# Kernel tuning notes

Measured on AMD Instinct MI355X. Metric: run time of the kernel, lower is better.

Reference implementation:

```python
import jax, jax.numpy as jnp
import numpy as np

EMBED_DIM = 1024
PROJ_DIM = 64
B, S = 8, 2048


def setup_inputs() -> dict:
    key = jax.random.key(0)
    k1, k2, k3 = jax.random.split(key, 3)
    context = jax.random.normal(k1, (S, B, EMBED_DIM), dtype=jnp.float32)
    prior = jax.random.uniform(k2, (B, S), dtype=jnp.float32)
    # xavier_uniform for (2*proj_dim, embed_dim)
    bound = float(np.sqrt(6.0 / (2 * PROJ_DIM + EMBED_DIM)))
    proj_weight = jax.random.uniform(k3, (2 * PROJ_DIM, EMBED_DIM), dtype=jnp.float32,
                                     minval=-bound, maxval=bound)
    proj_bias = jnp.zeros((2 * PROJ_DIM,), dtype=jnp.float32)
    return {"context": context, "prior": prior,
            "proj_weight": proj_weight, "proj_bias": proj_bias}


def reference(context, prior, proj_weight, proj_bias):
    # context: (S, B, E) -> (B, S, E)
    x = jnp.transpose(context, (1, 0, 2))
    b, s, e = x.shape
    qk = jnp.einsum('bse,pe->bsp', x, proj_weight) + proj_bias  # (B,S,2P)
    query, key = jnp.split(qk, 2, axis=2)
    # neighbor scores, scaled by embed_dim (as in the original)
    fwd = jnp.sum(query[:, :-1] * key[:, 1:], axis=-1) / e   # (B,S-1) score i<->i+1
    bwd = jnp.sum(query[:, 1:] * key[:, :-1], axis=-1) / e   # (B,S-1) score i<->i-1
    ninf = jnp.full((b, 1), -jnp.inf, dtype=x.dtype)
    score = jnp.stack([jnp.concatenate([fwd, ninf], axis=1),
                       jnp.concatenate([ninf, bwd], axis=1)], axis=-1)  # (B,S,2)
    prob = jax.nn.softmax(score, axis=-1)
    # torch .roll(shifts=-1) with no dims flattens the whole tensor: reproduce that
    shift_prob = jnp.roll(prob[:, :, 1].reshape(-1), -1).reshape(b, s)
    prob0 = jnp.sqrt(prob[:, :, 0] * shift_prob + 1e-6)      # (B,S)
    neighbor_attn = prior + (1.0 - prior) * prob0
    log_prob = jnp.log(neighbor_attn)
    # Original places log_prob[:, :-1] on the superdiagonal and hits it with
    # triu matmuls on both sides: C[i,j] = sum_{m=i}^{j-1} log_prob[m] for j>i.
    # Equivalent O(n^2): prefix sums cs[t] = sum_{m<t} log_prob[m].
    cs = jnp.concatenate([jnp.zeros((b, 1), dtype=x.dtype),
                          jnp.cumsum(log_prob[:, :-1], axis=1)], axis=1)  # (B,S)
    D = cs[:, None, :] - cs[:, :, None]            # D[b,i,j] = cs[j]-cs[i]
    i_idx = jnp.arange(s)
    upper = i_idx[None, :] > i_idx[:, None]        # (S,S) j>i
    M = jnp.where(upper[None], D, -D)              # C + C^T (symmetric)
    constituent_attn = jnp.exp(M)
    diag = i_idx[None, :] == i_idx[:, None]
    constituent_attn = jnp.where(diag[None], jnp.zeros((), x.dtype), constituent_attn)
    return constituent_attn, neighbor_attn
```

## Files before the change

kernel.cpp:

```cpp
#include <hip/hip_runtime.h>
#include <cstdint>
#include <cstddef>

#define E_DIM 1024
#define PD 64
#define NP 128
#define B_DIM 8
#define S_DIM 2048
#define M_TOT (B_DIM * S_DIM)

#define BMR 32
#define BK 32
#define NCH (E_DIM / BK)

typedef __attribute__((ext_vector_type(8))) short short8v;
typedef __attribute__((ext_vector_type(4))) float f32x4;

__device__ __forceinline__ void gload16(const void* g, void* l) {
    __builtin_amdgcn_global_load_lds(
        (const __attribute__((address_space(1))) unsigned int*)g,
        (__attribute__((address_space(3))) unsigned int*)(uintptr_t)l,
        16, 0, 0);
}

__device__ __forceinline__ void cvt_hilo(const f32x4 v0, const f32x4 v1,
                                         short8v& h, short8v& l) {
    const unsigned MSK = 0xFFFF0000u;
    unsigned a0 = __float_as_uint(v0.x), a1 = __float_as_uint(v0.y);
    unsigned a2 = __float_as_uint(v0.z), a3 = __float_as_uint(v0.w);
    unsigned a4 = __float_as_uint(v1.x), a5 = __float_as_uint(v1.y);
    unsigned a6 = __float_as_uint(v1.z), a7 = __float_as_uint(v1.w);
    float l0 = v0.x - __uint_as_float(a0 & MSK);
    float l1 = v0.y - __uint_as_float(a1 & MSK);
    float l2 = v0.z - __uint_as_float(a2 & MSK);
    float l3 = v0.w - __uint_as_float(a3 & MSK);
    float l4 = v1.x - __uint_as_float(a4 & MSK);
    float l5 = v1.y - __uint_as_float(a5 & MSK);
    float l6 = v1.z - __uint_as_float(a6 & MSK);
    float l7 = v1.w - __uint_as_float(a7 & MSK);
    union { unsigned u[4]; short8v s; } H, L;
    H.u[0] = (a1 & MSK) | (a0 >> 16);
    H.u[1] = (a3 & MSK) | (a2 >> 16);
    H.u[2] = (a5 & MSK) | (a4 >> 16);
    H.u[3] = (a7 & MSK) | (a6 >> 16);
    L.u[0] = (__float_as_uint(l1) & MSK) | (__float_as_uint(l0) >> 16);
    L.u[1] = (__float_as_uint(l3) & MSK) | (__float_as_uint(l2) >> 16);
    L.u[2] = (__float_as_uint(l5) & MSK) | (__float_as_uint(l4) >> 16);
    L.u[3] = (__float_as_uint(l7) & MSK) | (__float_as_uint(l6) >> 16);
    h = H.s; l = L.s;
}

__global__ __launch_bounds__(256) void conv_w(const float* __restrict__ W,
                                              ushort* __restrict__ hiImg,
                                              ushort* __restrict__ loImg) {
    const int t = blockIdx.x * 256 + threadIdx.x;
    const int c  = t & 127;
    const int q  = (t >> 7) & 3;
    const int ch = t >> 9;
    const float* src = W + (size_t)c * E_DIM + ch * 32 + q * 8;
    const f32x4 v0 = *(const f32x4*)src;
    const f32x4 v1 = *(const f32x4*)(src + 4);
    short8v h, l;
    cvt_hilo(v0, v1, h, l);
    const size_t off = ((size_t)(ch * 4 + q) * NP + c) * 8;
    *(short8v*)&hiImg[off] = h;
    *(short8v*)&loImg[off] = l;
}

__global__ __launch_bounds__(256, 2) void gemm_qk(const float* __restrict__ A,
                                                  const ushort* __restrict__ hiImg,
                                                  const ushort* __restrict__ loImg,
                                                  const float* __restrict__ bias,
                                                  float* __restrict__ qk) {
    __shared__ __align__(16) float  As[2][BMR][BK];
    __shared__ __align__(16) ushort Whi[2][4][NP][8];
    __shared__ __align__(16) ushort Wlo[2][4][NP][8];
    const int tid = threadIdx.x;
    const int m0  = blockIdx.x * BMR;
    const int w   = __builtin_amdgcn_readfirstlane(tid >> 6);
    const int ln  = tid & 63;
    const int lr  = ln >> 3;
    const int g8  = ln & 7;
    const int row16 = ln & 15;
    const int kq    = ln >> 4;
    const int r7    = row16 & 7;
    const int sg0 = ((((kq << 1) | 0) ^ r7) & 7) << 2;
    const int sg1 = ((((kq << 1) | 1) ^ r7) & 7) << 2;

    const float*  aS = A + (size_t)(m0 + w * 8 + lr) * E_DIM + ((g8 ^ lr) << 2);
    const ushort* hS = hiImg + (size_t)(w * 2) * 512 + ln * 8;
    const ushort* lS = loImg + (size_t)(w * 2) * 512 + ln * 8;

    float bias2[2];
    bias2[0] = bias[w * 32 + row16];
    bias2[1] = bias[w * 32 + 16 + row16];

    f32x4 acc[2][2];
#pragma unroll
    for (int i = 0; i < 2; ++i)
#pragma unroll
        for (int j = 0; j < 2; ++j) acc[i][j] = (f32x4){0.f, 0.f, 0.f, 0.f};

#define STAGE(BUF, CH)                                                          \
    {                                                                           \
        gload16(aS + (size_t)(CH) * BK, &As[BUF][w * 8][0]);                    \
        gload16(hS + (size_t)(CH) * 4096,       (ushort*)Whi[BUF] + (w * 2) * 512);       \
        gload16(hS + (size_t)(CH) * 4096 + 512, (ushort*)Whi[BUF] + (w * 2 + 1) * 512);   \
        gload16(lS + (size_t)(CH) * 4096,       (ushort*)Wlo[BUF] + (w * 2) * 512);       \
        gload16(lS + (size_t)(CH) * 4096 + 512, (ushort*)Wlo[BUF] + (w * 2 + 1) * 512);   \
    }

    STAGE(0, 0)

    for (int ch = 0; ch < NCH; ++ch) {
        const int buf = ch & 1;
        __syncthreads();
        if (ch + 1 < NCH) {
            STAGE(buf ^ 1, ch + 1)
        }
        short8v ah[2], al[2];
#pragma unroll
        for (int fi = 0; fi < 2; ++fi) {
            const float* base = &As[buf][fi * 16 + row16][0];
            const f32x4 v0 = *(const f32x4*)(base + sg0);
            const f32x4 v1 = *(const f32x4*)(base + sg1);
            cvt_hilo(v0, v1, ah[fi], al[fi]);
        }
        short8v wh[2], wl[2];
#pragma unroll
        for (int fj = 0; fj < 2; ++fj) {
            wh[fj] = *(const short8v*)&Whi[buf][kq][w * 32 + fj * 16 + row16][0];
            wl[fj] = *(const short8v*)&Wlo[buf][kq][w * 32 + fj * 16 + row16][0];
        }
#pragma unroll
        for (int fi = 0; fi < 2; ++fi)
#pragma unroll
            for (int fj = 0; fj < 2; ++fj) {
                acc[fi][fj] = __builtin_amdgcn_mfma_f32_16x16x32_bf16(
                    ah[fi], wh[fj], acc[fi][fj], 0, 0, 0);
                acc[fi][fj] = __builtin_amdgcn_mfma_f32_16x16x32_bf16(
                    ah[fi], wl[fj], acc[fi][fj], 0, 0, 0);
                acc[fi][fj] = __builtin_amdgcn_mfma_f32_16x16x32_bf16(
                    al[fi], wh[fj], acc[fi][fj], 0, 0, 0);
            }
    }
#undef STAGE

#pragma unroll
    for (int fi = 0; fi < 2; ++fi)
#pragma unroll
        for (int fj = 0; fj < 2; ++fj) {
#pragma unroll
            for (int r = 0; r < 4; ++r) {
                const int m = m0 + fi * 16 + kq * 4 + r;
                const int p = w * 32 + fj * 16 + row16;
                qk[(size_t)m * NP + p] = acc[fi][fj][r] + bias2[fj];
            }
        }
}

__global__ __launch_bounds__(256) void neighbor_probs(const float* __restrict__ qk,
                                                      float* __restrict__ p0,
                                                      float* __restrict__ p1) {
    const int m = blockIdx.x * 4 + (threadIdx.x >> 6);
    const int lane = threadIdx.x & 63;
    const int s = m >> 3;
    const int b = m & 7;

    const float q = qk[(size_t)m * NP + lane];
    const float kn = (s < S_DIM - 1) ? qk[(size_t)(m + B_DIM) * NP + PD + lane] : 0.f;
    const float kp = (s > 0) ? qk[(size_t)(m - B_DIM) * NP + PD + lane] : 0.f;
    float f = q * kn;
    float g = q * kp;
#pragma unroll
    for (int off = 32; off; off >>= 1) {
        f += __shfl_xor(f, off);
        g += __shfl_xor(g, off);
    }
    if (lane == 0) {
        const float s0 = f * (1.f / (float)E_DIM);
        const float s1 = g * (1.f / (float)E_DIM);
        float P0, P1;
        if (s == S_DIM - 1) { P0 = 0.f; P1 = 1.f; }
        else if (s == 0)    { P0 = 1.f; P1 = 0.f; }
        else {
            const float mx = fmaxf(s0, s1);
            const float e0 = __expf(s0 - mx), e1 = __expf(s1 - mx);
            const float inv = 1.f / (e0 + e1);
            P0 = e0 * inv; P1 = e1 * inv;
        }
        p0[b * S_DIM + s] = P0;
        p1[b * S_DIM + s] = P1;
    }
}

__global__ __launch_bounds__(256) void combine_scan(const float* __restrict__ p0,
                                                    const float* __restrict__ p1,
                                                    const float* __restrict__ prior,
                                                    float* __restrict__ out_na,
                                                    float* __restrict__ cs) {
    const int b = blockIdx.x;
    const int tid = threadIdx.x;
    __shared__ float sh[256];

    const int base = b * S_DIM + tid * 8;
    float incl[8];
    float run = 0.f;
#pragma unroll
    for (int u = 0; u < 8; ++u) {
        const int fidx = base + u;
        int nf = fidx + 1;
        if (nf == B_DIM * S_DIM) nf = 0;
        const float P0 = p0[fidx];
        const float sp = p1[nf];
        const float pr = prior[fidx];
        const float na = pr + (1.f - pr) * sqrtf(P0 * sp + 1e-6f);
        out_na[fidx] = na;
        run += __logf(na);
        incl[u] = run;
    }
    sh[tid] = run;
    __syncthreads();
    for (int off = 1; off < 256; off <<= 1) {
        float v = sh[tid];
        if (tid >= off) v += sh[tid - off];
        __syncthreads();
        sh[tid] = v;
        __syncthreads();
    }
    const float offset = (tid > 0) ? sh[tid - 1] : 0.f;
#pragma unroll
    for (int u = 0; u < 8; ++u) {
        cs[base + u] = offset + ((u > 0) ? incl[u - 1] : 0.f);
    }
}

__global__ __launch_bounds__(256) void big_out(const float* __restrict__ cs,
                                               float* __restrict__ out) {
    const int bi = blockIdx.x;
    const int b = bi >> 11;
    const int i = bi & (S_DIM - 1);
    const float ci = cs[b * S_DIM + i];
    const float* crow = cs + (size_t)b * S_DIM;
    float* orow = out + (size_t)bi * S_DIM;
    const int j0 = threadIdx.x * 8;
#pragma unroll
    for (int h = 0; h < 2; ++h) {
        const int j = j0 + h * 4;
        const f32x4 cj = *(const f32x4*)&crow[j];
        f32x4 o;
        {
            const int jj = j + 0; const float m = (jj > i) ? (cj.x - ci) : (ci - cj.x);
            o.x = (jj == i) ? 0.f : __expf(m);
        }
        {
            const int jj = j + 1; const float m = (jj > i) ? (cj.y - ci) : (ci - cj.y);
            o.y = (jj == i) ? 0.f : __expf(m);
        }
        {
            const int jj = j + 2; const float m = (jj > i) ? (cj.z - ci) : (ci - cj.z);
            o.z = (jj == i) ? 0.f : __expf(m);
        }
        {
            const int jj = j + 3; const float m = (jj > i) ? (cj.w - ci) : (ci - cj.w);
            o.w = (jj == i) ? 0.f : __expf(m);
        }
        *(f32x4*)&orow[j] = o;
    }
}

extern "C" void kernel_launch(void* const* d_in, const int* in_sizes, int n_in,
                              void* d_out, int out_size, void* d_ws, size_t ws_size,
                              hipStream_t stream) {
    const float* context = (const float*)d_in[0];
    const float* prior   = (const float*)d_in[1];
    const float* W       = (const float*)d_in[2];
    const float* bias    = (const float*)d_in[3];
    float* out = (float*)d_out;

    float* qk = (float*)d_ws;
    float* p0 = qk + (size_t)M_TOT * NP;
    float* p1 = p0 + M_TOT;
    float* cs = p1 + M_TOT;
    ushort* hiImg = (ushort*)out;
    ushort* loImg = hiImg + (size_t)NP * E_DIM;
    float* na_out = out + (size_t)B_DIM * S_DIM * S_DIM;

    conv_w<<<64, 256, 0, stream>>>(W, hiImg, loImg);
    gemm_qk<<<M_TOT / BMR, 256, 0, stream>>>(context, hiImg, loImg, bias, qk);
    neighbor_probs<<<M_TOT / 4, 256, 0, stream>>>(qk, p0, p1);
    combine_scan<<<B_DIM, 256, 0, stream>>>(p0, p1, prior, na_out, cs);
    big_out<<<M_TOT, 256, 0, stream>>>(cs, out);
}
```

Baseline: 64.49 us.

## Load weight images straight to registers and stage A through registers

Swaps the LDS-DMA (global_load_lds) double buffering for register prefetching. The hi/lo weight fragments are now read from global memory straight into registers two chunks ahead. A rows are loaded into registers and written by hand into a swizzled LDS double buffer. This drops the weight LDS arrays and their LDS reads, which lowers LDS traffic and footprint. The cost is more registers, manual waitcnt/sched barriers, and weight loads that each wave repeats from global memory (L2), with the usual risks of hand-written synchronisation.

```diff
diff --git a/kernel.cpp b/kernel.cpp
--- a/kernel.cpp
+++ b/kernel.cpp
@@ -15,13 +15,6 @@
 
 typedef __attribute__((ext_vector_type(8))) short short8v;
 typedef __attribute__((ext_vector_type(4))) float f32x4;
-
-__device__ __forceinline__ void gload16(const void* g, void* l) {
-    __builtin_amdgcn_global_load_lds(
-        (const __attribute__((address_space(1))) unsigned int*)g,
-        (__attribute__((address_space(3))) unsigned int*)(uintptr_t)l,
-        16, 0, 0);
-}
 
 __device__ __forceinline__ void cvt_hilo(const f32x4 v0, const f32x4 v1,
                                          short8v& h, short8v& l) {
@@ -72,12 +65,10 @@
                                                   const ushort* __restrict__ loImg,
                                                   const float* __restrict__ bias,
                                                   float* __restrict__ qk) {
-    __shared__ __align__(16) float  As[2][BMR][BK];
-    __shared__ __align__(16) ushort Whi[2][4][NP][8];
-    __shared__ __align__(16) ushort Wlo[2][4][NP][8];
+    __shared__ __align__(16) float As[2][BMR][BK];
     const int tid = threadIdx.x;
     const int m0  = blockIdx.x * BMR;
-    const int w   = __builtin_amdgcn_readfirstlane(tid >> 6);
+    const int w   = tid >> 6;
     const int ln  = tid & 63;
     const int lr  = ln >> 3;
     const int g8  = ln & 7;
@@ -87,9 +78,11 @@
     const int sg0 = ((((kq << 1) | 0) ^ r7) & 7) << 2;
     const int sg1 = ((((kq << 1) | 1) ^ r7) & 7) << 2;
 
-    const float*  aS = A + (size_t)(m0 + w * 8 + lr) * E_DIM + ((g8 ^ lr) << 2);
-    const ushort* hS = hiImg + (size_t)(w * 2) * 512 + ln * 8;
-    const ushort* lS = loImg + (size_t)(w * 2) * 512 + ln * 8;
+    const float* aS = A + (size_t)(m0 + w * 8 + lr) * E_DIM + (g8 << 2);
+    float* const aDst0 = &As[0][0][0] + (w * 8 + lr) * BK + ((g8 ^ lr) << 2);
+    float* const aDst1 = &As[1][0][0] + (w * 8 + lr) * BK + ((g8 ^ lr) << 2);
+    const ushort* hS = hiImg + ((size_t)kq * NP + w * 32 + row16) * 8;
+    const ushort* lS = loImg + ((size_t)kq * NP + w * 32 + row16) * 8;
 
     float bias2[2];
     bias2[0] = bias[w * 32 + row16];
@@ -101,50 +94,69 @@
 #pragma unroll
         for (int j = 0; j < 2; ++j) acc[i][j] = (f32x4){0.f, 0.f, 0.f, 0.f};
 
-#define STAGE(BUF, CH)                                                          \
-    {                                                                           \
-        gload16(aS + (size_t)(CH) * BK, &As[BUF][w * 8][0]);                    \
-        gload16(hS + (size_t)(CH) * 4096,       (ushort*)Whi[BUF] + (w * 2) * 512);       \
-        gload16(hS + (size_t)(CH) * 4096 + 512, (ushort*)Whi[BUF] + (w * 2 + 1) * 512);   \
-        gload16(lS + (size_t)(CH) * 4096,       (ushort*)Wlo[BUF] + (w * 2) * 512);       \
-        gload16(lS + (size_t)(CH) * 4096 + 512, (ushort*)Wlo[BUF] + (w * 2 + 1) * 512);   \
-    }
-
-    STAGE(0, 0)
-
-    for (int ch = 0; ch < NCH; ++ch) {
-        const int buf = ch & 1;
-        __syncthreads();
-        if (ch + 1 < NCH) {
-            STAGE(buf ^ 1, ch + 1)
-        }
-        short8v ah[2], al[2];
-#pragma unroll
-        for (int fi = 0; fi < 2; ++fi) {
-            const float* base = &As[buf][fi * 16 + row16][0];
-            const f32x4 v0 = *(const f32x4*)(base + sg0);
-            const f32x4 v1 = *(const f32x4*)(base + sg1);
-            cvt_hilo(v0, v1, ah[fi], al[fi]);
-        }
-        short8v wh[2], wl[2];
-#pragma unroll
-        for (int fj = 0; fj < 2; ++fj) {
-            wh[fj] = *(const short8v*)&Whi[buf][kq][w * 32 + fj * 16 + row16][0];
-            wl[fj] = *(const short8v*)&Wlo[buf][kq][w * 32 + fj * 16 + row16][0];
-        }
-#pragma unroll
-        for (int fi = 0; fi < 2; ++fi)
-#pragma unroll
-            for (int fj = 0; fj < 2; ++fj) {
-                acc[fi][fj] = __builtin_amdgcn_mfma_f32_16x16x32_bf16(
-                    ah[fi], wh[fj], acc[fi][fj], 0, 0, 0);
-                acc[fi][fj] = __builtin_amdgcn_mfma_f32_16x16x32_bf16(
-                    ah[fi], wl[fj], acc[fi][fj], 0, 0, 0);
-                acc[fi][fj] = __builtin_amdgcn_mfma_f32_16x16x32_bf16(
-                    al[fi], wh[fj], acc[fi][fj], 0, 0, 0);
-            }
-    }
-#undef STAGE
+    f32x4 aP0, aP1;
+    short8v wh00, wh01, wl00, wl01;
+    short8v wh10, wh11, wl10, wl11;
+
+    aP0 = *(const f32x4*)(aS);
+    aP1 = *(const f32x4*)(aS + BK);
+    wh00 = *(const short8v*)(hS);
+    wh01 = *(const short8v*)(hS + 128);
+    wl00 = *(const short8v*)(lS);
+    wl01 = *(const short8v*)(lS + 128);
+    wh10 = *(const short8v*)(hS + 4096);
+    wh11 = *(const short8v*)(hS + 4096 + 128);
+    wl10 = *(const short8v*)(lS + 4096);
+    wl11 = *(const short8v*)(lS + 4096 + 128);
+    *(f32x4*)aDst0 = aP0;
+    asm volatile("s_waitcnt lgkmcnt(0)" ::: "memory");
+    __builtin_amdgcn_sched_barrier(0);
+
+#define GBODY(P, CH, APcur, APother, WH0, WH1, WL0, WL1, DSTother, SRCbuf)          \
+    {                                                                               \
+        __builtin_amdgcn_s_barrier();                                               \
+        __builtin_amdgcn_sched_barrier(0);                                          \
+        if ((CH) + 1 < NCH) { *(f32x4*)(DSTother) = APother; }                      \
+        if ((CH) + 2 < NCH) {                                                       \
+            APcur = *(const f32x4*)(aS + ((CH) + 2) * BK);                          \
+        }                                                                           \
+        short8v ah0, al0, ah1, al1;                                                 \
+        {                                                                           \
+            const float* b0 = &As[SRCbuf][row16][0];                                \
+            cvt_hilo(*(const f32x4*)(b0 + sg0), *(const f32x4*)(b0 + sg1), ah0, al0); \
+            const float* b1 = &As[SRCbuf][16 + row16][0];                           \
+            cvt_hilo(*(const f32x4*)(b1 + sg0), *(const f32x4*)(b1 + sg1), ah1, al1); \
+        }                                                                           \
+        acc[0][0] = __builtin_amdgcn_mfma_f32_16x16x32_bf16(ah0, WH0, acc[0][0], 0, 0, 0); \
+        acc[0][0] = __builtin_amdgcn_mfma_f32_16x16x32_bf16(ah0, WL0, acc[0][0], 0, 0, 0); \
+        acc[0][0] = __builtin_amdgcn_mfma_f32_16x16x32_bf16(al0, WH0, acc[0][0], 0, 0, 0); \
+        acc[0][1] = __builtin_amdgcn_mfma_f32_16x16x32_bf16(ah0, WH1, acc[0][1], 0, 0, 0); \
+        acc[0][1] = __builtin_amdgcn_mfma_f32_16x16x32_bf16(ah0, WL1, acc[0][1], 0, 0, 0); \
+        acc[0][1] = __builtin_amdgcn_mfma_f32_16x16x32_bf16(al0, WH1, acc[0][1], 0, 0, 0); \
+        acc[1][0] = __builtin_amdgcn_mfma_f32_16x16x32_bf16(ah1, WH0, acc[1][0], 0, 0, 0); \
+        acc[1][0] = __builtin_amdgcn_mfma_f32_16x16x32_bf16(ah1, WL0, acc[1][0], 0, 0, 0); \
+        acc[1][0] = __builtin_amdgcn_mfma_f32_16x16x32_bf16(al1, WH0, acc[1][0], 0, 0, 0); \
+        acc[1][1] = __builtin_amdgcn_mfma_f32_16x16x32_bf16(ah1, WH1, acc[1][1], 0, 0, 0); \
+        acc[1][1] = __builtin_amdgcn_mfma_f32_16x16x32_bf16(ah1, WL1, acc[1][1], 0, 0, 0); \
+        acc[1][1] = __builtin_amdgcn_mfma_f32_16x16x32_bf16(al1, WH1, acc[1][1], 0, 0, 0); \
+        if ((CH) + 2 < NCH) {                                                       \
+            WH0 = *(const short8v*)(hS + (size_t)((CH) + 2) * 4096);                \
+            WH1 = *(const short8v*)(hS + (size_t)((CH) + 2) * 4096 + 128);          \
+            WL0 = *(const short8v*)(lS + (size_t)((CH) + 2) * 4096);                \
+            WL1 = *(const short8v*)(lS + (size_t)((CH) + 2) * 4096 + 128);          \
+        }                                                                           \
+        asm volatile("s_waitcnt lgkmcnt(0)" ::: "memory");                          \
+        __builtin_amdgcn_sched_barrier(0);                                          \
+    }
+
+#pragma unroll 1
+    for (int c2 = 0; c2 < NCH / 2; ++c2) {
+        const int ch0 = 2 * c2;
+        GBODY(0, ch0, aP0, aP1, wh00, wh01, wl00, wl01, aDst1, 0)
+        const int ch1 = 2 * c2 + 1;
+        GBODY(1, ch1, aP1, aP0, wh10, wh11, wl10, wl11, aDst0, 1)
+    }
+#undef GBODY
 
 #pragma unroll
     for (int fi = 0; fi < 2; ++fi)
```

Result: slower. 66.23 us (+2.7%).

## Fuse all stages into one cooperative persistent kernel with grid syncs

Applied to the files above, without the earlier changes.

Replaces the five separate launches (weight conversion, GEMM, neighbor probs, scan, big output) with a single cooperative kernel of 512 blocks separated by grid.sync. The GEMM tile now loads 48 rows (with 8-row halos) so neighbor dot products are computed from LDS without writing the full qk matrix to global memory. Weights are read directly from global into registers instead of LDS staging, and the output phase caches the cs row in LDS with each block writing 32 rows. This trades launch overhead and qk round-trips for redundant halo GEMM work, grid-wide barriers, and an only partly occupied scan phase.

```diff
diff --git a/kernel.cpp b/kernel.cpp
--- a/kernel.cpp
+++ b/kernel.cpp
@@ -1,6 +1,9 @@
 #include <hip/hip_runtime.h>
+#include <hip/hip_cooperative_groups.h>
 #include <cstdint>
 #include <cstddef>
+
+namespace cg = cooperative_groups;
 
 #define E_DIM 1024
 #define PD 64
@@ -9,9 +12,9 @@
 #define S_DIM 2048
 #define M_TOT (B_DIM * S_DIM)
 
-#define BMR 32
 #define BK 32
 #define NCH (E_DIM / BK)
+#define GRID 512
 
 typedef __attribute__((ext_vector_type(8))) short short8v;
 typedef __attribute__((ext_vector_type(4))) float f32x4;
@@ -50,222 +53,240 @@
     h = H.s; l = L.s;
 }
 
-__global__ __launch_bounds__(256) void conv_w(const float* __restrict__ W,
-                                              ushort* __restrict__ hiImg,
-                                              ushort* __restrict__ loImg) {
-    const int t = blockIdx.x * 256 + threadIdx.x;
-    const int c  = t & 127;
-    const int q  = (t >> 7) & 3;
-    const int ch = t >> 9;
-    const float* src = W + (size_t)c * E_DIM + ch * 32 + q * 8;
-    const f32x4 v0 = *(const f32x4*)src;
-    const f32x4 v1 = *(const f32x4*)(src + 4);
-    short8v h, l;
-    cvt_hilo(v0, v1, h, l);
-    const size_t off = ((size_t)(ch * 4 + q) * NP + c) * 8;
-    *(short8v*)&hiImg[off] = h;
-    *(short8v*)&loImg[off] = l;
-}
-
-__global__ __launch_bounds__(256, 2) void gemm_qk(const float* __restrict__ A,
-                                                  const ushort* __restrict__ hiImg,
-                                                  const ushort* __restrict__ loImg,
-                                                  const float* __restrict__ bias,
-                                                  float* __restrict__ qk) {
-    __shared__ __align__(16) float  As[2][BMR][BK];
-    __shared__ __align__(16) ushort Whi[2][4][NP][8];
-    __shared__ __align__(16) ushort Wlo[2][4][NP][8];
+#define MFMA(d, a, b) d = __builtin_amdgcn_mfma_f32_16x16x32_bf16(a, b, d, 0, 0, 0)
+
+__global__ __launch_bounds__(256, 2) void fused_all(const float* __restrict__ A,
+                                                    const float* __restrict__ W,
+                                                    const float* __restrict__ prior,
+                                                    const float* __restrict__ bias,
+                                                    float* __restrict__ out,
+                                                    void* __restrict__ ws) {
+    __shared__ __align__(16) union {
+        struct { float As[2][48][BK]; float Cmat[48][132]; } b;
+        float csL[S_DIM];
+        float scan[256];
+    } sh;
+
+    ushort* hiImg = (ushort*)ws;
+    ushort* loImg = hiImg + (size_t)NP * E_DIM;
+    float*  wsf   = (float*)ws;
+    float*  p0    = wsf + 131072;
+    float*  p1    = p0 + M_TOT;
+    float*  cs    = p1 + M_TOT;
+    float*  na_out = out + (size_t)B_DIM * S_DIM * S_DIM;
+
     const int tid = threadIdx.x;
-    const int m0  = blockIdx.x * BMR;
-    const int w   = __builtin_amdgcn_readfirstlane(tid >> 6);
-    const int ln  = tid & 63;
-    const int lr  = ln >> 3;
-    const int g8  = ln & 7;
-    const int row16 = ln & 15;
-    const int kq    = ln >> 4;
-    const int r7    = row16 & 7;
-    const int sg0 = ((((kq << 1) | 0) ^ r7) & 7) << 2;
-    const int sg1 = ((((kq << 1) | 1) ^ r7) & 7) << 2;
-
-    const float*  aS = A + (size_t)(m0 + w * 8 + lr) * E_DIM + ((g8 ^ lr) << 2);
-    const ushort* hS = hiImg + (size_t)(w * 2) * 512 + ln * 8;
-    const ushort* lS = loImg + (size_t)(w * 2) * 512 + ln * 8;
-
-    float bias2[2];
-    bias2[0] = bias[w * 32 + row16];
-    bias2[1] = bias[w * 32 + 16 + row16];
-
-    f32x4 acc[2][2];
-#pragma unroll
-    for (int i = 0; i < 2; ++i)
-#pragma unroll
-        for (int j = 0; j < 2; ++j) acc[i][j] = (f32x4){0.f, 0.f, 0.f, 0.f};
-
-#define STAGE(BUF, CH)                                                          \
-    {                                                                           \
-        gload16(aS + (size_t)(CH) * BK, &As[BUF][w * 8][0]);                    \
-        gload16(hS + (size_t)(CH) * 4096,       (ushort*)Whi[BUF] + (w * 2) * 512);       \
-        gload16(hS + (size_t)(CH) * 4096 + 512, (ushort*)Whi[BUF] + (w * 2 + 1) * 512);   \
-        gload16(lS + (size_t)(CH) * 4096,       (ushort*)Wlo[BUF] + (w * 2) * 512);       \
-        gload16(lS + (size_t)(CH) * 4096 + 512, (ushort*)Wlo[BUF] + (w * 2 + 1) * 512);   \
+    const int g   = blockIdx.x;
+    cg::grid_group grid = cg::this_grid();
+
+    {
+        const int t = g * 256 + tid;
+        if (t < NP * E_DIM / 8) {
+            const int c  = t & 127;
+            const int q  = (t >> 7) & 3;
+            const int ch = t >> 9;
+            const float* src = W + (size_t)c * E_DIM + ch * 32 + q * 8;
+            const f32x4 v0 = *(const f32x4*)src;
+            const f32x4 v1 = *(const f32x4*)(src + 4);
+            short8v h, l;
+            cvt_hilo(v0, v1, h, l);
+            const size_t off = ((size_t)(ch * 4 + q) * NP + c) * 8;
+            *(short8v*)&hiImg[off] = h;
+            *(short8v*)&loImg[off] = l;
+        }
     }
-
-    STAGE(0, 0)
-
-    for (int ch = 0; ch < NCH; ++ch) {
-        const int buf = ch & 1;
+    grid.sync();
+
+    {
+        const int m0 = g * 32;
+        const int w  = tid >> 6;
+        const int ln = tid & 63;
+        const int lr = ln >> 3;
+        const int g8 = ln & 7;
+        const int row16 = ln & 15;
+        const int kq    = ln >> 4;
+        const int r7    = row16 & 7;
+        const int sg0 = ((((kq << 1) | 0) ^ r7) & 7) << 2;
+        const int sg1 = ((((kq << 1) | 1) ^ r7) & 7) << 2;
+
+        long gr1 = (long)m0 - 8 + w * 8 + lr;
+        gr1 = gr1 < 0 ? 0 : (gr1 >= M_TOT ? M_TOT - 1 : gr1);
+        const float* aP1 = A + (size_t)gr1 * E_DIM + ((g8 ^ lr) << 2);
+        const float* aP2 = aP1;
+        if (w < 2) {
+            long gr2 = (long)m0 - 8 + 32 + w * 8 + lr;
+            gr2 = gr2 < 0 ? 0 : (gr2 >= M_TOT ? M_TOT - 1 : gr2);
+            aP2 = A + (size_t)gr2 * E_DIM + ((g8 ^ lr) << 2);
+        }
+        const ushort* hS = hiImg + ((size_t)kq * NP + w * 32 + row16) * 8;
+        const ushort* lS = loImg + ((size_t)kq * NP + w * 32 + row16) * 8;
+        float bias2[2];
+        bias2[0] = bias[w * 32 + row16];
+        bias2[1] = bias[w * 32 + 16 + row16];
+
+        f32x4 acc[3][2];
+#pragma unroll
+        for (int i = 0; i < 3; ++i)
+#pragma unroll
+            for (int j = 0; j < 2; ++j) acc[i][j] = (f32x4){0.f, 0.f, 0.f, 0.f};
+
+        short8v whA0, whA1, wlA0, wlA1, whB0, whB1, wlB0, wlB1;
+
+        gload16(aP1, &sh.b.As[0][w * 8][0]);
+        if (w < 2) gload16(aP2, &sh.b.As[0][32 + w * 8][0]);
+        whA0 = *(const short8v*)(hS);
+        whA1 = *(const short8v*)(hS + 128);
+        wlA0 = *(const short8v*)(lS);
+        wlA1 = *(const short8v*)(lS + 128);
+
+#define GB(CH, WH0, WH1, WL0, WL1, NWH0, NWH1, NWL0, NWL1)                          \
+        {                                                                           \
+            const int buf = (CH) & 1;                                               \
+            __syncthreads();                                                        \
+            if ((CH) + 1 < NCH) {                                                   \
+                gload16(aP1 + ((CH) + 1) * BK, &sh.b.As[buf ^ 1][w * 8][0]);        \
+                if (w < 2) gload16(aP2 + ((CH) + 1) * BK, &sh.b.As[buf ^ 1][32 + w * 8][0]); \
+                NWH0 = *(const short8v*)(hS + (size_t)((CH) + 1) * 4096);           \
+                NWH1 = *(const short8v*)(hS + (size_t)((CH) + 1) * 4096 + 128);     \
+                NWL0 = *(const short8v*)(lS + (size_t)((CH) + 1) * 4096);           \
+                NWL1 = *(const short8v*)(lS + (size_t)((CH) + 1) * 4096 + 128);     \
+            }                                                                       \
+            short8v ah, al;                                                         \
+            _Pragma("unroll")                                                       \
+            for (int rf = 0; rf < 3; ++rf) {                                        \
+                const float* bp = &sh.b.As[buf][rf * 16 + row16][0];                \
+                cvt_hilo(*(const f32x4*)(bp + sg0), *(const f32x4*)(bp + sg1), ah, al); \
+                MFMA(acc[rf][0], ah, WH0);                                          \
+                MFMA(acc[rf][0], ah, WL0);                                          \
+                MFMA(acc[rf][0], al, WH0);                                          \
+                MFMA(acc[rf][1], ah, WH1);                                          \
+                MFMA(acc[rf][1], ah, WL1);                                          \
+                MFMA(acc[rf][1], al, WH1);                                          \
+            }                                                                       \
+        }
+
+#pragma unroll 1
+        for (int c2 = 0; c2 < NCH / 2; ++c2) {
+            GB(2 * c2,     whA0, whA1, wlA0, wlA1, whB0, whB1, wlB0, wlB1)
+            GB(2 * c2 + 1, whB0, whB1, wlB0, wlB1, whA0, whA1, wlA0, wlA1)
+        }
+#undef GB
+
         __syncthreads();
-        if (ch + 1 < NCH) {
-            STAGE(buf ^ 1, ch + 1)
-        }
-        short8v ah[2], al[2];
-#pragma unroll
-        for (int fi = 0; fi < 2; ++fi) {
-            const float* base = &As[buf][fi * 16 + row16][0];
-            const f32x4 v0 = *(const f32x4*)(base + sg0);
-            const f32x4 v1 = *(const f32x4*)(base + sg1);
-            cvt_hilo(v0, v1, ah[fi], al[fi]);
-        }
-        short8v wh[2], wl[2];
-#pragma unroll
-        for (int fj = 0; fj < 2; ++fj) {
-            wh[fj] = *(const short8v*)&Whi[buf][kq][w * 32 + fj * 16 + row16][0];
-            wl[fj] = *(const short8v*)&Wlo[buf][kq][w * 32 + fj * 16 + row16][0];
-        }
-#pragma unroll
-        for (int fi = 0; fi < 2; ++fi)
-#pragma unroll
-            for (int fj = 0; fj < 2; ++fj) {
-                acc[fi][fj] = __builtin_amdgcn_mfma_f32_16x16x32_bf16(
-                    ah[fi], wh[fj], acc[fi][fj], 0, 0, 0);
-                acc[fi][fj] = __builtin_amdgcn_mfma_f32_16x16x32_bf16(
-                    ah[fi], wl[fj], acc[fi][fj], 0, 0, 0);
-                acc[fi][fj] = __builtin_amdgcn_mfma_f32_16x16x32_bf16(
-                    al[fi], wh[fj], acc[fi][fj], 0, 0, 0);
+#pragma unroll
+        for (int rf = 0; rf < 3; ++rf)
+#pragma unroll
+            for (int fj = 0; fj < 2; ++fj)
+#pragma unroll
+                for (int r = 0; r < 4; ++r)
+                    sh.b.Cmat[rf * 16 + kq * 4 + r][w * 32 + fj * 16 + row16] =
+                        acc[rf][fj][r] + bias2[fj];
+        __syncthreads();
+
+#pragma unroll 1
+        for (int u = 0; u < 8; ++u) {
+            const int tr = 8 + w * 8 + u;
+            const float q  = sh.b.Cmat[tr][ln];
+            const float kf = sh.b.Cmat[tr + 8][64 + ln];
+            const float kb = sh.b.Cmat[tr - 8][64 + ln];
+            float f  = q * kf;
+            float g2 = q * kb;
+#pragma unroll
+            for (int off = 32; off; off >>= 1) {
+                f  += __shfl_xor(f, off);
+                g2 += __shfl_xor(g2, off);
             }
+            if (ln == 0) {
+                const int s_abs = g * 4 + w;
+                const int bb = u;
+                float P0, P1;
+                if (s_abs == 0)             { P0 = 1.f; P1 = 0.f; }
+                else if (s_abs == S_DIM - 1){ P0 = 0.f; P1 = 1.f; }
+                else {
+                    const float s0 = f  * (1.f / (float)E_DIM);
+                    const float s1 = g2 * (1.f / (float)E_DIM);
+                    const float mx = fmaxf(s0, s1);
+                    const float e0 = __expf(s0 - mx), e1 = __expf(s1 - mx);
+                    const float inv = 1.f / (e0 + e1);
+                    P0 = e0 * inv; P1 = e1 * inv;
+                }
+                p0[bb * S_DIM + s_abs] = P0;
+                p1[bb * S_DIM + s_abs] = P1;
+            }
+        }
     }
-#undef STAGE
-
-#pragma unroll
-    for (int fi = 0; fi < 2; ++fi)
-#pragma unroll
-        for (int fj = 0; fj < 2; ++fj) {
-#pragma unroll
-            for (int r = 0; r < 4; ++r) {
-                const int m = m0 + fi * 16 + kq * 4 + r;
-                const int p = w * 32 + fj * 16 + row16;
-                qk[(size_t)m * NP + p] = acc[fi][fj][r] + bias2[fj];
+    grid.sync();
+
+    if (g < B_DIM) {
+        const int b = g;
+        const int base = b * S_DIM + tid * 8;
+        float incl[8];
+        float run = 0.f;
+#pragma unroll
+        for (int u = 0; u < 8; ++u) {
+            const int fidx = base + u;
+            int nf = fidx + 1;
+            if (nf == B_DIM * S_DIM) nf = 0;
+            const float P0 = p0[fidx];
+            const float sp = p1[nf];
+            const float pr = prior[fidx];
+            const float na = pr + (1.f - pr) * sqrtf(P0 * sp + 1e-6f);
+            na_out[fidx] = na;
+            run += __logf(na);
+            incl[u] = run;
+        }
+        sh.scan[tid] = run;
+        __syncthreads();
+        for (int off = 1; off < 256; off <<= 1) {
+            float v = sh.scan[tid];
+            if (tid >= off) v += sh.scan[tid - off];
+            __syncthreads();
+            sh.scan[tid] = v;
+            __syncthreads();
+        }
+        const float offset = (tid > 0) ? sh.scan[tid - 1] : 0.f;
+#pragma unroll
+        for (int u = 0; u < 8; ++u) {
+            cs[base + u] = offset + ((u > 0) ? incl[u - 1] : 0.f);
+        }
+    }
+    grid.sync();
+
+    {
+        const int bD = g >> 6;
+        for (int j = tid; j < S_DIM; j += 256) sh.csL[j] = cs[bD * S_DIM + j];
+        __syncthreads();
+#pragma unroll 1
+        for (int r = 0; r < 32; ++r) {
+            const int rowg = g * 32 + r;
+            const int i = rowg & (S_DIM - 1);
+            const float ci = sh.csL[i];
+            float* orow = out + (size_t)rowg * S_DIM;
+            const int j0 = tid * 8;
+#pragma unroll
+            for (int h = 0; h < 2; ++h) {
+                const int j = j0 + h * 4;
+                const f32x4 cj = *(const f32x4*)&sh.csL[j];
+                f32x4 o;
+                {
+                    const int jj = j + 0; const float m = (jj > i) ? (cj.x - ci) : (ci - cj.x);
+                    o.x = (jj == i) ? 0.f : __expf(m);
+                }
+                {
+                    const int jj = j + 1; const float m = (jj > i) ? (cj.y - ci) : (ci - cj.y);
+                    o.y = (jj == i) ? 0.f : __expf(m);
+                }
+                {
+                    const int jj = j + 2; const float m = (jj > i) ? (cj.z - ci) : (ci - cj.z);
+                    o.z = (jj == i) ? 0.f : __expf(m);
+                }
+                {
+                    const int jj = j + 3; const float m = (jj > i) ? (cj.w - ci) : (ci - cj.w);
+                    o.w = (jj == i) ? 0.f : __expf(m);
+                }
+                *(f32x4*)&orow[j] = o;
             }
         }
-}
-
-__global__ __launch_bounds__(256) void neighbor_probs(const float* __restrict__ qk,
-                                                      float* __restrict__ p0,
-                                                      float* __restrict__ p1) {
-    const int m = blockIdx.x * 4 + (threadIdx.x >> 6);
-    const int lane = threadIdx.x & 63;
-    const int s = m >> 3;
-    const int b = m & 7;
-
-    const float q = qk[(size_t)m * NP + lane];
-    const float kn = (s < S_DIM - 1) ? qk[(size_t)(m + B_DIM) * NP + PD + lane] : 0.f;
-    const float kp = (s > 0) ? qk[(size_t)(m - B_DIM) * NP + PD + lane] : 0.f;
-    float f = q * kn;
-    float g = q * kp;
-#pragma unroll
-    for (int off = 32; off; off >>= 1) {
-        f += __shfl_xor(f, off);
-        g += __shfl_xor(g, off);
-    }
-    if (lane == 0) {
-        const float s0 = f * (1.f / (float)E_DIM);
-        const float s1 = g * (1.f / (float)E_DIM);
-        float P0, P1;
-        if (s == S_DIM - 1) { P0 = 0.f; P1 = 1.f; }
-        else if (s == 0)    { P0 = 1.f; P1 = 0.f; }
-        else {
-            const float mx = fmaxf(s0, s1);
-            const float e0 = __expf(s0 - mx), e1 = __expf(s1 - mx);
-            const float inv = 1.f / (e0 + e1);
-            P0 = e0 * inv; P1 = e1 * inv;
-        }
-        p0[b * S_DIM + s] = P0;
-        p1[b * S_DIM + s] = P1;
-    }
-}
-
-__global__ __launch_bounds__(256) void combine_scan(const float* __restrict__ p0,
-                                                    const float* __restrict__ p1,
-                                                    const float* __restrict__ prior,
-                                                    float* __restrict__ out_na,
-                                                    float* __restrict__ cs) {
-    const int b = blockIdx.x;
-    const int tid = threadIdx.x;
-    __shared__ float sh[256];
-
-    const int base = b * S_DIM + tid * 8;
-    float incl[8];
-    float run = 0.f;
-#pragma unroll
-    for (int u = 0; u < 8; ++u) {
-        const int fidx = base + u;
-        int nf = fidx + 1;
-        if (nf == B_DIM * S_DIM) nf = 0;
-        const float P0 = p0[fidx];
-        const float sp = p1[nf];
-        const float pr = prior[fidx];
-        const float na = pr + (1.f - pr) * sqrtf(P0 * sp + 1e-6f);
-        out_na[fidx] = na;
-        run += __logf(na);
-        incl[u] = run;
-    }
-    sh[tid] = run;
-    __syncthreads();
-    for (int off = 1; off < 256; off <<= 1) {
-        float v = sh[tid];
-        if (tid >= off) v += sh[tid - off];
-        __syncthreads();
-        sh[tid] = v;
-        __syncthreads();
-    }
-    const float offset = (tid > 0) ? sh[tid - 1] : 0.f;
-#pragma unroll
-    for (int u = 0; u < 8; ++u) {
-        cs[base + u] = offset + ((u > 0) ? incl[u - 1] : 0.f);
-    }
-}
-
-__global__ __launch_bounds__(256) void big_out(const float* __restrict__ cs,
-                                               float* __restrict__ out) {
-    const int bi = blockIdx.x;
-    const int b = bi >> 11;
-    const int i = bi & (S_DIM - 1);
-    const float ci = cs[b * S_DIM + i];
-    const float* crow = cs + (size_t)b * S_DIM;
-    float* orow = out + (size_t)bi * S_DIM;
-    const int j0 = threadIdx.x * 8;
-#pragma unroll
-    for (int h = 0; h < 2; ++h) {
-        const int j = j0 + h * 4;
-        const f32x4 cj = *(const f32x4*)&crow[j];
-        f32x4 o;
-        {
-            const int jj = j + 0; const float m = (jj > i) ? (cj.x - ci) : (ci - cj.x);
-            o.x = (jj == i) ? 0.f : __expf(m);
-        }
-        {
-            const int jj = j + 1; const float m = (jj > i) ? (cj.y - ci) : (ci - cj.y);
-            o.y = (jj == i) ? 0.f : __expf(m);
-        }
-        {
-            const int jj = j + 2; const float m = (jj > i) ? (cj.z - ci) : (ci - cj.z);
-            o.z = (jj == i) ? 0.f : __expf(m);
-        }
-        {
-            const int jj = j + 3; const float m = (jj > i) ? (cj.w - ci) : (ci - cj.w);
-            o.w = (jj == i) ? 0.f : __expf(m);
-        }
-        *(f32x4*)&orow[j] = o;
     }
 }
 
@@ -278,17 +299,8 @@
     const float* bias    = (const float*)d_in[3];
     float* out = (float*)d_out;
 
-    float* qk = (float*)d_ws;
-    float* p0 = qk + (size_t)M_TOT * NP;
-    float* p1 = p0 + M_TOT;
-    float* cs = p1 + M_TOT;
-    ushort* hiImg = (ushort*)out;
-    ushort* loImg = hiImg + (size_t)NP * E_DIM;
-    float* na_out = out + (size_t)B_DIM * S_DIM * S_DIM;
-
-    conv_w<<<64, 256, 0, stream>>>(W, hiImg, loImg);
-    gemm_qk<<<M_TOT / BMR, 256, 0, stream>>>(context, hiImg, loImg, bias, qk);
-    neighbor_probs<<<M_TOT / 4, 256, 0, stream>>>(qk, p0, p1);
-    combine_scan<<<B_DIM, 256, 0, stream>>>(p0, p1, prior, na_out, cs);
-    big_out<<<M_TOT, 256, 0, stream>>>(cs, out);
+    void* args[] = {(void*)&context, (void*)&W, (void*)&prior, (void*)&bias,
+                    (void*)&out, (void*)&d_ws};
+    hipLaunchCooperativeKernel((const void*)fused_all, dim3(GRID), dim3(256),
+                               args, 0, stream);
 }
```

New measurement: 214.0 us. 232% more time.
